# Optimization experiments

Hardware: AMD Instinct MI355X
Metric: run time of the kernel (lower is better)

## Reference

```python
import jax, jax.numpy as jnp
import numpy as np

B, N, NE = 16, 96, 256
ATOM, EDIM, HID, LAT, HEADS = 128, 16, 128, 128, 4
HD = LAT // HEADS
RBF, CUT, ZEMB, MAXZ = 16, 5.0, 32, 100
MUL0_IN, MUL1_IN = 64, 32      # irreps_node = 64x0e + 32x1o (dim 160)
MUL0_OUT, MUL1_OUT = 32, 16    # out irreps  = 32x0e + 16x1o (dim 80)
NODE_DIM = MUL0_IN + 3 * MUL1_IN
OUT_DIM = MUL0_OUT + 3 * MUL1_OUT
E_ATT = 1024
WNUM = MUL0_IN*MUL0_OUT + MUL0_IN*MUL1_OUT + MUL1_IN*MUL1_OUT + MUL1_IN*MUL0_OUT  # 4608


def _mlp3(x, w1, b1, w2, b2, w3, b3):
    x = jax.nn.silu(x @ w1 + b1)
    x = jax.nn.silu(x @ w2 + b2)
    return x @ w3 + b3


def setup_inputs() -> dict:
    key = jax.random.key(0)
    ks = jax.random.split(key, 40)
    s = 0.05  # scale params so deep MLP activations stay numerically sane
    d = {}
    d['h'] = jax.random.normal(ks[0], (B, N, ATOM), jnp.float32)
    d['h_full'] = jax.random.normal(ks[1], (B, N, NODE_DIM), jnp.float32)
    d['e_feat'] = jax.random.normal(ks[2], (NE, EDIM), jnp.float32)
    d['att_dist'] = jax.random.uniform(ks[3], (E_ATT,), jnp.float32)
    d['att_vec'] = jax.random.normal(ks[4], (E_ATT, 3), jnp.float32)
    d['z_emb_table'] = jax.random.normal(ks[5], (MAXZ + 1, ZEMB), jnp.float32) * s
    d['rw1'] = jax.random.normal(ks[6], (ZEMB + 1 + RBF, HID), jnp.float32) * s
    d['rb1'] = jnp.zeros((HID,), jnp.float32)
    d['rw2'] = jax.random.normal(ks[7], (HID, WNUM), jnp.float32) * s
    d['rb2'] = jnp.zeros((WNUM,), jnp.float32)
    d['ew1'] = jax.random.normal(ks[8], (EDIM, HID), jnp.float32) * s
    d['eb1'] = jnp.zeros((HID,), jnp.float32)
    d['ew2'] = jax.random.normal(ks[9], (HID, MUL0_OUT + MUL1_OUT), jnp.float32) * s
    d['eb2'] = jnp.zeros((MUL0_OUT + MUL1_OUT,), jnp.float32)
    d['qw1'] = jax.random.normal(ks[10], (ATOM + EDIM, HID), jnp.float32) * s
    d['qb1'] = jnp.zeros((HID,), jnp.float32)
    d['qw2'] = jax.random.normal(ks[11], (HID, HID), jnp.float32) * s
    d['qb2'] = jnp.zeros((HID,), jnp.float32)
    d['qw3'] = jax.random.normal(ks[12], (HID, LAT), jnp.float32) * s
    d['qb3'] = jnp.zeros((LAT,), jnp.float32)
    d['kw1'] = jax.random.normal(ks[13], (ATOM + ZEMB + 1 + RBF, HID), jnp.float32) * s
    d['kb1'] = jnp.zeros((HID,), jnp.float32)
    d['kw2'] = jax.random.normal(ks[14], (HID, HID), jnp.float32) * s
    d['kb2'] = jnp.zeros((HID,), jnp.float32)
    d['kw3'] = jax.random.normal(ks[15], (HID, LAT), jnp.float32) * s
    d['kb3'] = jnp.zeros((LAT,), jnp.float32)
    d['ow1'] = jax.random.normal(ks[16], (MUL0_OUT + MUL1_OUT, HID), jnp.float32) * s
    d['ob1'] = jnp.zeros((HID,), jnp.float32)
    d['ow2'] = jax.random.normal(ks[17], (HID, HID), jnp.float32) * s
    d['ob2'] = jnp.zeros((HID,), jnp.float32)
    d['ow3'] = jax.random.normal(ks[18], (HID, LAT), jnp.float32) * s
    d['ob3'] = jnp.zeros((LAT,), jnp.float32)
    d['z'] = jax.random.randint(ks[19], (B, N), 0, MAXZ)
    d['mask'] = jnp.ones((B, N), bool)
    d['absorber_index'] = jax.random.randint(ks[20], (B,), 0, N)
    d['att_dst'] = jnp.arange(E_ATT)  # unique flat indices into B*N
    return d


def reference(h, h_full, e_feat, att_dist, att_vec, z_emb_table,
              rw1, rb1, rw2, rb2, ew1, eb1, ew2, eb2,
              qw1, qb1, qw2, qb2, qw3, qb3,
              kw1, kb1, kw2, kb2, kw3, kb3,
              ow1, ob1, ow2, ob2, ow3, ob3,
              z, mask, absorber_index, att_dst):
    Bz, Na, Hd = h.shape
    F = Bz * Na
    nE = e_feat.shape[0]
    # scatter edge data into flat (B*N) atom slots
    am_flat = jnp.zeros((F,), bool).at[att_dst].set(True)
    d_flat = jnp.zeros((F,), h.dtype).at[att_dst].set(att_dist)
    v_flat = jnp.zeros((F, 3), h.dtype).at[att_dst].set(att_vec)
    att_mask = am_flat.reshape(Bz, Na) & mask
    # spherical harmonics (lmax=1, component normalization): Y0 = 1, Y1 = sqrt(3)*unit_vec
    un = v_flat / jnp.maximum(jnp.linalg.norm(v_flat, axis=-1, keepdims=True), 1e-8)
    y1 = jnp.sqrt(3.0) * un
    # Gaussian RBF on absorber->atom distance
    mu = jnp.linspace(0.0, CUT, RBF)
    delta = CUT / (RBF - 1)
    rbf = jnp.exp(-(d_flat[:, None] - mu) ** 2 / (2.0 * delta * delta))  # (F, RBF)
    zr = z_emb_table[z]                      # (B, N, ZEMB)
    zr_flat = zr.reshape(F, -1)
    is_abs = jnp.zeros((Bz, Na), h.dtype).at[jnp.arange(Bz), absorber_index].set(1.0)
    # radial MLP -> per-edge tensor-product weights
    w_in = jnp.concatenate([zr_flat, is_abs.reshape(F, 1), rbf], -1)
    tpw = jax.nn.silu(w_in @ rw1 + rb1) @ rw2 + rb2  # (F, WNUM)
    s1 = MUL0_IN * MUL0_OUT
    s2 = s1 + MUL0_IN * MUL1_OUT
    s3 = s2 + MUL1_IN * MUL1_OUT
    w00 = tpw[:, :s1].reshape(F, MUL0_IN, MUL0_OUT)   # 0e x 0e -> 0e
    w01 = tpw[:, s1:s2].reshape(F, MUL0_IN, MUL1_OUT) # 0e x 1o -> 1o
    w10 = tpw[:, s2:s3].reshape(F, MUL1_IN, MUL1_OUT) # 1o x 0e -> 1o
    w11 = tpw[:, s3:].reshape(F, MUL1_IN, MUL0_OUT)   # 1o x 1o -> 0e
    hf = h_full.reshape(F, -1)
    x0 = hf[:, :MUL0_IN]
    x1 = hf[:, MUL0_IN:].reshape(F, MUL1_IN, 3)
    alpha = 1.0 / jnp.sqrt(jnp.float32(MUL0_IN + MUL1_IN))  # path fan-in normalization
    c = 1.0 / jnp.sqrt(3.0)                                  # wigner-3j coeff for l=1 couplings
    out0 = alpha * (jnp.einsum('fi,fio->fo', x0, w00)
                    + c * jnp.einsum('fim,fm,fio->fo', x1, y1, w11))
    out1 = alpha * c * (jnp.einsum('fi,fm,fio->fom', x0, y1, w01)
                        + jnp.einsum('fim,fio->fom', x1, w10))
    v_irrep = jnp.concatenate([out0, out1.reshape(F, 3 * MUL1_OUT)], -1)  # (F, OUT_DIM)
    # cosine cutoff envelope + edge mask
    env = jnp.where(d_flat < CUT, 0.5 * (jnp.cos(jnp.pi * d_flat / CUT) + 1.0), 0.0)
    v_irrep = v_irrep * (am_flat.astype(h.dtype) * env)[:, None]
    # energy-conditioned per-irrep-channel modulation
    gates = jax.nn.silu(e_feat @ ew1 + eb1) @ ew2 + eb2  # (nE, 48)
    g_exp = jnp.concatenate([gates[:, :MUL0_OUT],
                             jnp.repeat(gates[:, MUL0_OUT:], 3, axis=-1)], -1)  # (nE, OUT_DIM)
    v_mod = (v_irrep[:, None, :] * g_exp[None]).reshape(Bz, Na, nE, OUT_DIM)
    # invariant multi-head scoring
    h_abs = h[jnp.arange(Bz), absorber_index]  # (B, H)
    q_in = jnp.concatenate([jnp.broadcast_to(h_abs[:, None], (Bz, nE, Hd)),
                            jnp.broadcast_to(e_feat[None], (Bz, nE, EDIM))], -1)
    q = _mlp3(q_in, qw1, qb1, qw2, qb2, qw3, qb3)  # (B, nE, LAT)
    atom_static = jnp.concatenate([h, zr, is_abs[..., None], rbf.reshape(Bz, Na, RBF)], -1)
    k = _mlp3(atom_static, kw1, kb1, kw2, kb2, kw3, kb3)  # (B, N, LAT)
    qh = q.reshape(Bz, nE, HEADS, HD)
    kh = k.reshape(Bz, Na, HEADS, HD)
    scores = (jnp.einsum('behd,bnhd->benh', qh, kh) * (HD ** -0.5)).mean(-1)  # (B, nE, N)
    m = att_mask[:, None, :]
    scores = jnp.where(m, scores, -1e9)
    attn = jax.nn.softmax(scores, axis=2) * m.astype(h.dtype)
    attn = attn / jnp.maximum(attn.sum(2, keepdims=True), 1e-8)
    out_irrep = jnp.einsum('ben,bnec->bec', attn, v_mod)  # (B, nE, OUT_DIM)
    # invariants: scalars + vector norms
    scal = out_irrep[..., :MUL0_OUT]
    vec = out_irrep[..., MUL0_OUT:].reshape(Bz, nE, MUL1_OUT, 3)
    inv = jnp.concatenate([scal, jnp.sqrt(jnp.sum(vec * vec, -1) + 1e-12)], -1)
    return _mlp3(inv, ow1, ob1, ow2, ob2, ow3, ob3)  # (B, nE, LAT)
```

## Files before the change

### kernel.cpp

```cpp
#include <hip/hip_runtime.h>
#include <hip/hip_fp16.h>
#include <math.h>

#define BB 16
#define NN 96
#define NE 256
#define FF (BB*NN)
#define ATOM 128
#define EDIM 16
#define HID 128
#define LAT 128
#define RBFN 16
#define CUTOFF 5.0f
#define ZEMB 32
#define E_ATT 1024
#define M0I 64
#define M1I 32
#define M0O 32
#define M1O 16
#define NODE_DIM 160
#define OUT_DIM 80
#define INVD 48
#define WNUM 4608
#define SEG1 2048
#define SEG2 3072
#define SEG3 3584

#define NODE_BLKS (FF/4)
#define EC_BLKS 16
#define HABS_BLKS 2
#define GATE_BLKS 16
#define TRANS_BLKS 144
#define STAGE1_BLKS (NODE_BLKS + EC_BLKS + HABS_BLKS + GATE_BLKS + TRANS_BLKS)

#define MFMA_BLKS (36*16)
#define MQ_BLKS (MFMA_BLKS + 512)

#define SCORE_BLKS 128
#define ST_BLKS (SCORE_BLKS + 512)

typedef _Float16 half8_t __attribute__((ext_vector_type(8)));
typedef float float4v __attribute__((ext_vector_type(4)));

__device__ __forceinline__ float silu_f(float x) { return x / (1.0f + expf(-x)); }

__global__ __launch_bounds__(1024) void k_prep(
    const int* __restrict__ att_dst, const float* __restrict__ att_dist,
    const float* __restrict__ att_vec,
    int* __restrict__ inv, float* __restrict__ y1E, float* __restrict__ envE)
{
    int t = threadIdx.x;
    inv[t] = -1;
    if (t < FF - 1024) inv[1024 + t] = -1;
    {
        float d = att_dist[t];
        envE[t] = (d < CUTOFF) ? 0.5f*(cosf(3.14159265358979323846f*d/CUTOFF) + 1.0f) : 0.0f;
        float vx = att_vec[3*t], vy = att_vec[3*t+1], vz = att_vec[3*t+2];
        float nrm = sqrtf(vx*vx + vy*vy + vz*vz);
        float is = 1.0f / fmaxf(nrm, 1e-8f);
        const float s3 = 1.7320508075688772f;
        y1E[3*t]   = s3*vx*is;
        y1E[3*t+1] = s3*vy*is;
        y1E[3*t+2] = s3*vz*is;
    }
    __syncthreads();
    inv[att_dst[t]] = t;
}

__global__ __launch_bounds__(256) void k_stage1(
    const float* __restrict__ h, const float* __restrict__ z_emb, const int* __restrict__ z,
    const int* __restrict__ absorber, const float* __restrict__ e_feat,
    const int* __restrict__ inv, const float* __restrict__ att_dist,
    const float* __restrict__ rw1, const float* __restrict__ rb1,
    const float* __restrict__ kw1, const float* __restrict__ kb1,
    const float* __restrict__ kw2, const float* __restrict__ kb2,
    const float* __restrict__ kw3, const float* __restrict__ kb3,
    const float* __restrict__ qw1,
    const float* __restrict__ ew1, const float* __restrict__ eb1,
    const float* __restrict__ ew2, const float* __restrict__ eb2,
    const float* __restrict__ rw2,
    __half* __restrict__ hiddenH, float* __restrict__ kmatw,
    float* __restrict__ ecw, float* __restrict__ habs1w, float* __restrict__ gexp,
    __half* __restrict__ rw2T)
{
    __shared__ float smem[3488];
    int blk = blockIdx.x;
    int t = threadIdx.x;

    if (blk < NODE_BLKS) {
        float (*sin1)[184] = (float(*)[184])smem;
        float (*l1S)[128]  = (float(*)[128])(smem + 736);
        float (*l2S)[128]  = (float(*)[128])(smem + 736 + 512);
        int f0 = blk * 4;
        {
            int n = t >> 6, i2 = t & 63;
            float2 hv = *(const float2*)&h[(f0 + n)*ATOM + i2*2];
            sin1[n][i2*2] = hv.x; sin1[n][i2*2 + 1] = hv.y;
        }
        if (t < 128) {
            int n = t >> 5, j = t & 31;
            sin1[n][ATOM + j] = z_emb[z[f0 + n]*ZEMB + j];
        }
        if (t < 64) {
            int n = t >> 4, j = t & 15;
            int e = inv[f0 + n];
            float d = ((unsigned)e < E_ATT) ? att_dist[e] : 0.0f;
            const float delta = CUTOFF / (RBFN - 1);
            float diff = d - j*delta;
            sin1[n][ATOM + ZEMB + 1 + j] = expf(-diff*diff / (2.0f*delta*delta));
        }
        if (t < 4) {
            int f = f0 + t;
            int b = f / NN, nn = f - b*NN;
            sin1[t][ATOM + ZEMB] = (absorber[b] == nn) ? 1.0f : 0.0f;
        }
        __syncthreads();
        int n = t >> 6;
        int c2 = (t & 63) * 2;
        int e = inv[f0 + n];
        bool att_ = ((unsigned)e < E_ATT);
        if (att_) {
            float2 a0 = *(const float2*)&rb1[c2];
            float2 a1 = make_float2(0.f, 0.f);
            #pragma unroll 8
            for (int i = 0; i < 48; i += 2) {
                float x0v = sin1[n][ATOM + i], x1v = sin1[n][ATOM + i + 1];
                float2 w0 = *(const float2*)&rw1[i*HID + c2];
                float2 w1 = *(const float2*)&rw1[(i+1)*HID + c2];
                a0.x += x0v*w0.x; a0.y += x0v*w0.y;
                a1.x += x1v*w1.x; a1.y += x1v*w1.y;
            }
            {
                float x0v = sin1[n][ATOM + 48];
                float2 w0 = *(const float2*)&rw1[48*HID + c2];
                a0.x += x0v*w0.x; a0.y += x0v*w0.y;
            }
            *(__half2*)&hiddenH[e*HID + c2] =
                __floats2half2_rn(silu_f(a0.x + a1.x), silu_f(a0.y + a1.y));
        }
        if (att_) {
            float2 a0 = *(const float2*)&kb1[c2];
            float2 a1 = make_float2(0.f, 0.f);
            #pragma unroll 8
            for (int i = 0; i < 176; i += 2) {
                float x0v = sin1[n][i], x1v = sin1[n][i + 1];
                float2 w0 = *(const float2*)&kw1[i*HID + c2];
                float2 w1 = *(const float2*)&kw1[(i+1)*HID + c2];
                a0.x += x0v*w0.x; a0.y += x0v*w0.y;
                a1.x += x1v*w1.x; a1.y += x1v*w1.y;
            }
            {
                float x0v = sin1[n][176];
                float2 w0 = *(const float2*)&kw1[176*HID + c2];
                a0.x += x0v*w0.x; a0.y += x0v*w0.y;
            }
            l1S[n][c2] = silu_f(a0.x + a1.x); l1S[n][c2+1] = silu_f(a0.y + a1.y);
        }
        __syncthreads();
        if (att_) {
            float2 a0 = *(const float2*)&kb2[c2];
            float2 a1 = make_float2(0.f, 0.f);
            #pragma unroll 8
            for (int i = 0; i < HID; i += 2) {
                float x0v = l1S[n][i], x1v = l1S[n][i + 1];
                float2 w0 = *(const float2*)&kw2[i*HID + c2];
                float2 w1 = *(const float2*)&kw2[(i+1)*HID + c2];
                a0.x += x0v*w0.x; a0.y += x0v*w0.y;
                a1.x += x1v*w1.x; a1.y += x1v*w1.y;
            }
            l2S[n][c2] = silu_f(a0.x + a1.x); l2S[n][c2+1] = silu_f(a0.y + a1.y);
        }
        __syncthreads();
        if (att_) {
            float2 a0 = *(const float2*)&kb3[c2];
            float2 a1 = make_float2(0.f, 0.f);
            #pragma unroll 8
            for (int i = 0; i < HID; i += 2) {
                float x0v = l2S[n][i], x1v = l2S[n][i + 1];
                float2 w0 = *(const float2*)&kw3[i*HID + c2];
                float2 w1 = *(const float2*)&kw3[(i+1)*HID + c2];
                a0.x += x0v*w0.x; a0.y += x0v*w0.y;
                a1.x += x1v*w1.x; a1.y += x1v*w1.y;
            }
            float2 o; o.x = a0.x + a1.x; o.y = a0.y + a1.y;
            *(float2*)&kmatw[(f0 + n)*HID + c2] = o;
        }
    } else if (blk < NODE_BLKS + EC_BLKS) {
        float (*ef)[16] = (float(*)[16])smem;
        int e0 = (blk - NODE_BLKS) * 16;
        { int e = t >> 4, i = t & 15; ef[e][i] = e_feat[(e0 + e)*EDIM + i]; }
        __syncthreads();
        int r = t >> 4, c0 = (t & 15)*8;
        float4 a0 = make_float4(0,0,0,0), a1 = a0;
        #pragma unroll
        for (int i = 0; i < EDIM; i++) {
            float a = ef[r][i];
            float4 w0 = *(const float4*)&qw1[(ATOM + i)*HID + c0];
            float4 w1 = *(const float4*)&qw1[(ATOM + i)*HID + c0 + 4];
            a0.x += a*w0.x; a0.y += a*w0.y; a0.z += a*w0.z; a0.w += a*w0.w;
            a1.x += a*w1.x; a1.y += a*w1.y; a1.z += a*w1.z; a1.w += a*w1.w;
        }
        *(float4*)&ecw[(e0 + r)*HID + c0] = a0;
        *(float4*)&ecw[(e0 + r)*HID + c0 + 4] = a1;
    } else if (blk < NODE_BLKS + EC_BLKS + HABS_BLKS) {
        float (*hr)[128] = (float(*)[128])smem;
        int b0 = (blk - NODE_BLKS - EC_BLKS) * 8;
        {
            int r = t >> 5, i4 = t & 31;
            int b = b0 + r;
            int a = absorber[b];
            *(float4*)&hr[r][i4*4] = *(const float4*)&h[(b*NN + a)*ATOM + i4*4];
        }
        __syncthreads();
        int r = t >> 5, c0 = (t & 31)*4;
        float4 a0 = make_float4(0,0,0,0), a1 = a0;
        #pragma unroll 8
        for (int i = 0; i < ATOM; i += 2) {
            float x0v = hr[r][i], x1v = hr[r][i+1];
            float4 w0 = *(const float4*)&qw1[i*HID + c0];
            float4 w1 = *(const float4*)&qw1[(i+1)*HID + c0];
            a0.x += x0v*w0.x; a0.y += x0v*w0.y; a0.z += x0v*w0.z; a0.w += x0v*w0.w;
            a1.x += x1v*w1.x; a1.y += x1v*w1.y; a1.z += x1v*w1.z; a1.w += x1v*w1.w;
        }
        float4 o;
        o.x = a0.x + a1.x; o.y = a0.y + a1.y; o.z = a0.z + a1.z; o.w = a0.w + a1.w;
        *(float4*)&habs1w[(b0 + r)*HID + c0] = o;
    } else if (blk < NODE_BLKS + EC_BLKS + HABS_BLKS + GATE_BLKS) {
        float (*ef)[16]   = (float(*)[16])smem;
        float (*l1g)[128] = (float(*)[128])(smem + 256);
        float (*gg)[48]   = (float(*)[48])(smem + 256 + 2048);
        int e0 = (blk - NODE_BLKS - EC_BLKS - HABS_BLKS) * 16;
        { int e = t >> 4, i = t & 15; ef[e][i] = e_feat[(e0 + e)*EDIM + i]; }
        __syncthreads();
        int r = t >> 4, c0 = (t & 15)*8;
        {
            float4 a0 = *(const float4*)&eb1[c0];
            float4 a1 = *(const float4*)&eb1[c0 + 4];
            #pragma unroll
            for (int i = 0; i < EDIM; i++) {
                float a = ef[r][i];
                float4 w0 = *(const float4*)&ew1[i*HID + c0];
                float4 w1 = *(const float4*)&ew1[i*HID + c0 + 4];
                a0.x += a*w0.x; a0.y += a*w0.y; a0.z += a*w0.z; a0.w += a*w0.w;
                a1.x += a*w1.x; a1.y += a*w1.y; a1.z += a*w1.z; a1.w += a*w1.w;
            }
            l1g[r][c0]   = silu_f(a0.x); l1g[r][c0+1] = silu_f(a0.y);
            l1g[r][c0+2] = silu_f(a0.z); l1g[r][c0+3] = silu_f(a0.w);
            l1g[r][c0+4] = silu_f(a1.x); l1g[r][c0+5] = silu_f(a1.y);
            l1g[r][c0+6] = silu_f(a1.z); l1g[r][c0+7] = silu_f(a1.w);
        }
        __syncthreads();
        for (int u = t; u < 16*48; u += 256) {
            int e = u / 48, j = u - 48*(u/48);
            float acc = eb2[j];
            #pragma unroll 4
            for (int i = 0; i < HID; i++) acc += l1g[e][i]*ew2[i*48 + j];
            gg[e][j] = acc;
        }
        __syncthreads();
        for (int u = t; u < 16*80; u += 256) {
            int e = u / 80, cc = u - 80*(u/80);
            gexp[(e0 + e)*OUT_DIM + cc] = (cc < M0O) ? gg[e][cc] : gg[e][M0O + (cc - M0O)/3];
        }
    } else {
        __half* lds = (__half*)smem;
        int tb = blk - (NODE_BLKS + EC_BLKS + HABS_BLKS + GATE_BLKS);
        int nt = tb % 72, kt = tb / 72;
        int n0 = nt*64, k0 = kt*64;
        for (int p = 0; p < 16; p++) {
            int idx = t + 256*p;
            int kk = idx >> 6, nn = idx & 63;
            lds[nn*66 + kk] = __float2half(rw2[(k0+kk)*WNUM + n0+nn]);
        }
        __syncthreads();
        for (int p = 0; p < 16; p++) {
            int idx = t + 256*p;
            int nn = idx >> 6, kk = idx & 63;
            rw2T[(n0+nn)*HID + k0+kk] = lds[nn*66 + kk];
        }
    }
}

__global__ __launch_bounds__(256) void k_mq(
    const __half* __restrict__ hiddenH, const __half* __restrict__ rw2T,
    const float* __restrict__ rb2,
    const float* __restrict__ habs1, const float* __restrict__ ec, const float* __restrict__ qb1,
    const float* __restrict__ qw2, const float* __restrict__ qb2,
    const float* __restrict__ qw3, const float* __restrict__ qb3,
    __half* __restrict__ tpwE, float* __restrict__ qmat)
{
    __shared__ __align__(16) char smemraw[17408];
    int blk = blockIdx.x;
    int t = threadIdx.x;
    if (blk < MFMA_BLKS) {
        int colTile = blk % 36;
        int rowGrp  = blk / 36;
        int wv = t >> 6;
        int lane = t & 63;
        int m0 = (rowGrp*4 + wv) * 16;
        int n0 = colTile * 128;
        int mrow = lane & 15, quad = lane >> 4;
        __half* cS = (__half*)smemraw + wv * (16*136);
        const _Float16* hp = (const _Float16*)hiddenH + (m0 + mrow)*HID + quad*8;
        half8_t af[4];
        #pragma unroll
        for (int kc = 0; kc < 4; kc++) af[kc] = *(const half8_t*)(hp + kc*32);
        #pragma unroll
        for (int nt = 0; nt < 8; nt++) {
            const _Float16* bp = (const _Float16*)rw2T + (n0 + nt*16 + mrow)*HID + quad*8;
            float4v acc = {0.f, 0.f, 0.f, 0.f};
            #pragma unroll
            for (int kc = 0; kc < 4; kc++) {
                half8_t bf = *(const half8_t*)(bp + kc*32);
                acc = __builtin_amdgcn_mfma_f32_16x16x32_f16(af[kc], bf, acc, 0, 0, 0);
            }
            float bias = rb2[n0 + nt*16 + mrow];
            #pragma unroll
            for (int r = 0; r < 4; r++)
                cS[(quad*4 + r)*136 + nt*16 + mrow] = __float2half(acc[r] + bias);
        }
        #pragma unroll
        for (int p = 0; p < 4; p++) {
            int chunk = lane + 64*p;
            int row = chunk >> 4, c8 = (chunk & 15)*8;
            float4 v = *(float4*)&cS[row*136 + c8];
            *(float4*)&tpwE[(long)(m0 + row)*WNUM + n0 + c8] = v;
        }
    } else {
        float* l1S = (float*)smemraw;
        float* l2S = (float*)smemraw + 1024;
        int r0 = (blk - MFMA_BLKS) * 8;
        for (int p = 0; p < 4; p++) {
            int idx = t + 256*p;
            int rr = idx >> 7, i = idx & 127;
            int be = r0 + rr; int b = be >> 8; int e = be & 255;
            l1S[rr*128 + i] = silu_f(habs1[b*HID + i] + ec[e*HID + i] + qb1[i]);
        }
        __syncthreads();
        int r = t >> 5, c0 = (t & 31)*4;
        {
            float4 a0 = *(const float4*)&qb2[c0];
            float4 a1 = make_float4(0,0,0,0);
            #pragma unroll 8
            for (int i = 0; i < HID; i += 2) {
                float x0v = l1S[r*128 + i], x1v = l1S[r*128 + i+1];
                float4 w0 = *(const float4*)&qw2[i*HID + c0];
                float4 w1 = *(const float4*)&qw2[(i+1)*HID + c0];
                a0.x += x0v*w0.x; a0.y += x0v*w0.y; a0.z += x0v*w0.z; a0.w += x0v*w0.w;
                a1.x += x1v*w1.x; a1.y += x1v*w1.y; a1.z += x1v*w1.z; a1.w += x1v*w1.w;
            }
            l2S[r*128 + c0]   = silu_f(a0.x + a1.x); l2S[r*128 + c0+1] = silu_f(a0.y + a1.y);
            l2S[r*128 + c0+2] = silu_f(a0.z + a1.z); l2S[r*128 + c0+3] = silu_f(a0.w + a1.w);
        }
        __syncthreads();
        {
            float4 a0 = *(const float4*)&qb3[c0];
            float4 a1 = make_float4(0,0,0,0);
            #pragma unroll 8
            for (int i = 0; i < HID; i += 2) {
                float x0v = l2S[r*128 + i], x1v = l2S[r*128 + i+1];
                float4 w0 = *(const float4*)&qw3[i*HID + c0];
                float4 w1 = *(const float4*)&qw3[(i+1)*HID + c0];
                a0.x += x0v*w0.x; a0.y += x0v*w0.y; a0.z += x0v*w0.z; a0.w += x0v*w0.w;
                a1.x += x1v*w1.x; a1.y += x1v*w1.y; a1.z += x1v*w1.z; a1.w += x1v*w1.w;
            }
            float4 o;
            o.x = a0.x + a1.x; o.y = a0.y + a1.y; o.z = a0.z + a1.z; o.w = a0.w + a1.w;
            *(float4*)&qmat[(r0 + r)*LAT + c0] = o;
        }
    }
}

__global__ __launch_bounds__(256) void k_st(
    const float* __restrict__ qmat, const float* __restrict__ kmat, const int* __restrict__ inv,
    const float* __restrict__ h_full, const __half* __restrict__ tpwE,
    const int* __restrict__ att_dst,
    const float* __restrict__ envE, const float* __restrict__ y1E,
    float* __restrict__ scoresW, float* __restrict__ virr)
{
    __shared__ float smem[8544];
    int blk = blockIdx.x;
    int t = threadIdx.x;
    if (blk < SCORE_BLKS) {
        int b  = blk >> 3;
        int e0 = (blk & 7) * 32;
        float (*Qs)[132] = (float(*)[132])smem;
        float (*Kt)[132] = (float(*)[132])(smem + 32*132);
        float* mS = smem + 2*32*132;
        for (int p = 0; p < 4; p++) {
            int idx = t + 256*p; int e = idx >> 5, i4 = idx & 31;
            *(float4*)&Qs[e][i4*4] = *(const float4*)&qmat[(b*NE + e0 + e)*LAT + i4*4];
        }
        if (t < NN) mS[t] = ((unsigned)inv[b*NN + t] < E_ATT) ? 1.0f : 0.0f;
        int te = t >> 5, tn = t & 31;
        float acc[4][3] = {};
        for (int nt = 0; nt < 3; nt++) {
            __syncthreads();
            for (int p = 0; p < 4; p++) {
                int idx = t + 256*p; int n = idx >> 5, i4 = idx & 31;
                *(float4*)&Kt[n][i4*4] = *(const float4*)&kmat[(b*NN + nt*32 + n)*LAT + i4*4];
            }
            __syncthreads();
            for (int i = 0; i < LAT; i++) {
                float bv = Kt[tn][i];
                acc[0][nt] += Qs[te*4 + 0][i]*bv;
                acc[1][nt] += Qs[te*4 + 1][i]*bv;
                acc[2][nt] += Qs[te*4 + 2][i]*bv;
                acc[3][nt] += Qs[te*4 + 3][i]*bv;
            }
        }
        const float scale = 0.04419417382415922f;
        #pragma unroll
        for (int j = 0; j < 4; j++)
            #pragma unroll
            for (int jj = 0; jj < 3; jj++) {
                int n = tn + 32*jj;
                float s = (mS[n] != 0.f) ? acc[j][jj]*scale : -1e9f;
                scoresW[((b*NE) + e0 + te*4 + j)*NN + n] = s;
            }
    } else {
        int sub = t >> 7, tt = t & 127;
        int e = (blk - SCORE_BLKS)*2 + sub;
        int f = att_dst[e];
        float* x0  = smem + sub*256;
        float* x1f = smem + sub*256 + 64;
        float* xy  = smem + sub*256 + 160;
        float* y1s = smem + sub*256 + 192;
        const float* hf = h_full + f*NODE_DIM;
        if (tt < M0I) x0[tt] = hf[tt];
        if (tt < M1I*3) x1f[tt] = hf[M0I + tt];
        if (tt < 3) y1s[tt] = y1E[3*e + tt];
        __syncthreads();
        if (tt < M1I) xy[tt] = x1f[3*tt]*y1s[0] + x1f[3*tt+1]*y1s[1] + x1f[3*tt+2]*y1s[2];
        __syncthreads();
        float scale = envE[e];
        const __half* w = tpwE + (long)e*WNUM;
        const float alpha = 0.10206207261596575f;
        const float cc = 0.5773502691896258f;
        if (tt < M0O) {
            float t00 = 0.f, t11 = 0.f;
            #pragma unroll 4
            for (int i = 0; i < M0I; i++) t00 += x0[i]*__half2float(w[i*M0O + tt]);
            #pragma unroll 4
            for (int i = 0; i < M1I; i++) t11 += xy[i]*__half2float(w[SEG3 + i*M0O + tt]);
            virr[f*OUT_DIM + tt] = alpha*(t00 + cc*t11)*scale;
        } else if (tt < M0O + 3*M1O) {
            int idx = tt - M0O; int o = idx/3, m = idx - 3*o;
            float t01 = 0.f, t10 = 0.f;
            #pragma unroll 4
            for (int i = 0; i < M0I; i++) t01 += x0[i]*__half2float(w[SEG1 + i*M1O + o]);
            #pragma unroll 4
            for (int i = 0; i < M1I; i++) t10 += x1f[i*3 + m]*__half2float(w[SEG2 + i*M1O + o]);
            virr[f*OUT_DIM + tt] = alpha*cc*(t01*y1s[m] + t10)*scale;
        }
    }
}

__global__ __launch_bounds__(256) void k_attf(
    const float* __restrict__ scoresW, const int* __restrict__ inv,
    const float* __restrict__ virr, const float* __restrict__ gexp,
    const float* __restrict__ ow1, const float* __restrict__ ob1,
    const float* __restrict__ ow2, const float* __restrict__ ob2,
    const float* __restrict__ ow3, const float* __restrict__ ob3,
    float* __restrict__ out)
{
    int b  = blockIdx.x >> 5;
    int e0 = (blockIdx.x & 31) * 8;
    int t = threadIdx.x;
    __shared__ float aS[8][100];
    __shared__ float gS[8][84];
    __shared__ float ocS[8][84];
    __shared__ float mS[NN];
    __shared__ float inS[8][INVD];
    __shared__ float l1S[8][HID];
    __shared__ float l2S[8][HID];

    for (int p = 0; p < 3; p++) {
        int idx = t + 256*p;
        int el = idx / NN, n = idx - NN*(idx/NN);
        aS[el][n] = scoresW[((b*NE) + e0 + el)*NN + n];
    }
    if (t < 160) {
        int el = t / 20, c4 = t - 20*(t/20);
        *(float4*)&gS[el][c4*4] = *(const float4*)&gexp[(e0 + el)*OUT_DIM + c4*4];
    }
    if (t < NN) mS[t] = ((unsigned)inv[b*NN + t] < E_ATT) ? 1.0f : 0.0f;
    __syncthreads();

    {
        int el = t >> 5;
        int ng = t & 31;
        float s0 = aS[el][ng], s1 = aS[el][ng + 32], s2 = aS[el][ng + 64];
        float m0 = mS[ng], m1 = mS[ng + 32], m2 = mS[ng + 64];
        float mx = fmaxf(s0, fmaxf(s1, s2));
        #pragma unroll
        for (int off = 1; off < 32; off <<= 1) mx = fmaxf(mx, __shfl_xor(mx, off));
        float e0v = expf(s0 - mx), e1v = expf(s1 - mx), e2v = expf(s2 - mx);
        float sm = e0v + e1v + e2v;
        #pragma unroll
        for (int off = 1; off < 32; off <<= 1) sm += __shfl_xor(sm, off);
        float r = 1.0f / sm;
        float p0 = m0*e0v*r, p1 = m1*e1v*r, p2 = m2*e2v*r;
        float ss = p0 + p1 + p2;
        #pragma unroll
        for (int off = 1; off < 32; off <<= 1) ss += __shfl_xor(ss, off);
        float is = 1.0f / fmaxf(ss, 1e-8f);
        aS[el][ng]      = p0*is;
        aS[el][ng + 32] = p1*is;
        aS[el][ng + 64] = p2*is;
    }
    __syncthreads();

    if (t < 160) {
        int el = t / 20, c4 = t - 20*(t/20);
        const float* vp = virr + (long)b*NN*OUT_DIM + c4*4;
        float4 acc = make_float4(0,0,0,0);
        #pragma unroll 4
        for (int n = 0; n < NN; n++) {
            float a = aS[el][n];
            float4 v = *(const float4*)&vp[n*OUT_DIM];
            acc.x += a*v.x; acc.y += a*v.y; acc.z += a*v.z; acc.w += a*v.w;
        }
        float4 g = *(float4*)&gS[el][c4*4];
        float4 o; o.x = acc.x*g.x; o.y = acc.y*g.y; o.z = acc.z*g.z; o.w = acc.w*g.w;
        *(float4*)&ocS[el][c4*4] = o;
    }
    __syncthreads();

    for (int u = t; u < 8*INVD; u += 256) {
        int el = u / INVD, j = u - INVD*(u/INVD);
        float val;
        if (j < M0O) val = ocS[el][j];
        else {
            int o = j - M0O;
            float x = ocS[el][M0O + 3*o], y = ocS[el][M0O + 3*o + 1], zz = ocS[el][M0O + 3*o + 2];
            val = sqrtf(x*x + y*y + zz*zz + 1e-12f);
        }
        inS[el][j] = val;
    }
    __syncthreads();

    int r = t >> 5, c0 = (t & 31)*4;
    {
        float4 a0 = *(const float4*)&ob1[c0];
        float4 a1 = make_float4(0,0,0,0);
        #pragma unroll 8
        for (int i = 0; i < INVD; i += 2) {
            float x0v = inS[r][i], x1v = inS[r][i+1];
            float4 w0 = *(const float4*)&ow1[i*HID + c0];
            float4 w1 = *(const float4*)&ow1[(i+1)*HID + c0];
            a0.x += x0v*w0.x; a0.y += x0v*w0.y; a0.z += x0v*w0.z; a0.w += x0v*w0.w;
            a1.x += x1v*w1.x; a1.y += x1v*w1.y; a1.z += x1v*w1.z; a1.w += x1v*w1.w;
        }
        l1S[r][c0]   = silu_f(a0.x + a1.x); l1S[r][c0+1] = silu_f(a0.y + a1.y);
        l1S[r][c0+2] = silu_f(a0.z + a1.z); l1S[r][c0+3] = silu_f(a0.w + a1.w);
    }
    __syncthreads();
    {
        float4 a0 = *(const float4*)&ob2[c0];
        float4 a1 = make_float4(0,0,0,0);
        #pragma unroll 8
        for (int i = 0; i < HID; i += 2) {
            float x0v = l1S[r][i], x1v = l1S[r][i+1];
            float4 w0 = *(const float4*)&ow2[i*HID + c0];
            float4 w1 = *(const float4*)&ow2[(i+1)*HID + c0];
            a0.x += x0v*w0.x; a0.y += x0v*w0.y; a0.z += x0v*w0.z; a0.w += x0v*w0.w;
            a1.x += x1v*w1.x; a1.y += x1v*w1.y; a1.z += x1v*w1.z; a1.w += x1v*w1.w;
        }
        l2S[r][c0]   = silu_f(a0.x + a1.x); l2S[r][c0+1] = silu_f(a0.y + a1.y);
        l2S[r][c0+2] = silu_f(a0.z + a1.z); l2S[r][c0+3] = silu_f(a0.w + a1.w);
    }
    __syncthreads();
    {
        float4 a0 = *(const float4*)&ob3[c0];
        float4 a1 = make_float4(0,0,0,0);
        #pragma unroll 8
        for (int i = 0; i < HID; i += 2) {
            float x0v = l2S[r][i], x1v = l2S[r][i+1];
            float4 w0 = *(const float4*)&ow3[i*HID + c0];
            float4 w1 = *(const float4*)&ow3[(i+1)*HID + c0];
            a0.x += x0v*w0.x; a0.y += x0v*w0.y; a0.z += x0v*w0.z; a0.w += x0v*w0.w;
            a1.x += x1v*w1.x; a1.y += x1v*w1.y; a1.z += x1v*w1.z; a1.w += x1v*w1.w;
        }
        float4 o;
        o.x = a0.x + a1.x; o.y = a0.y + a1.y; o.z = a0.z + a1.z; o.w = a0.w + a1.w;
        *(float4*)&out[((b*NE + e0) + r)*LAT + c0] = o;
    }
}

extern "C" void kernel_launch(void* const* d_in, const int* in_sizes, int n_in,
                              void* d_out, int out_size, void* d_ws, size_t ws_size,
                              hipStream_t stream) {
    const float* h        = (const float*)d_in[0];
    const float* h_full   = (const float*)d_in[1];
    const float* e_feat   = (const float*)d_in[2];
    const float* att_dist = (const float*)d_in[3];
    const float* att_vec  = (const float*)d_in[4];
    const float* z_emb    = (const float*)d_in[5];
    const float* rw1 = (const float*)d_in[6];  const float* rb1 = (const float*)d_in[7];
    const float* rw2 = (const float*)d_in[8];  const float* rb2 = (const float*)d_in[9];
    const float* ew1 = (const float*)d_in[10]; const float* eb1 = (const float*)d_in[11];
    const float* ew2 = (const float*)d_in[12]; const float* eb2 = (const float*)d_in[13];
    const float* qw1 = (const float*)d_in[14]; const float* qb1 = (const float*)d_in[15];
    const float* qw2 = (const float*)d_in[16]; const float* qb2 = (const float*)d_in[17];
    const float* qw3 = (const float*)d_in[18]; const float* qb3 = (const float*)d_in[19];
    const float* kw1 = (const float*)d_in[20]; const float* kb1 = (const float*)d_in[21];
    const float* kw2 = (const float*)d_in[22]; const float* kb2 = (const float*)d_in[23];
    const float* kw3 = (const float*)d_in[24]; const float* kb3 = (const float*)d_in[25];
    const float* ow1 = (const float*)d_in[26]; const float* ob1 = (const float*)d_in[27];
    const float* ow2 = (const float*)d_in[28]; const float* ob2 = (const float*)d_in[29];
    const float* ow3 = (const float*)d_in[30]; const float* ob3 = (const float*)d_in[31];
    const int* z        = (const int*)d_in[32];
    const int* absorber = (const int*)d_in[34];
    const int* att_dst  = (const int*)d_in[35];

    float* ws = (float*)d_ws;
    int*   inv     = (int*)ws;
    float* y1E     = ws + 1536;
    float* envE    = ws + 4608;
    float* kmat    = ws + 5632;
    float* qmat    = ws + 202240;
    float* gexp    = ws + 726528;
    float* virr    = ws + 747008;
    float* habs1   = ws + 869888;
    float* ec      = ws + 871936;
    float* scoresW = ws + 904704;
    __half* tpwE   = (__half*)(ws + 1297920);
    __half* rw2T   = (__half*)(ws + 3657216);
    __half* hiddenH= (__half*)(ws + 3952128);

    float* out = (float*)d_out;

    k_prep<<<1, 1024, 0, stream>>>(att_dst, att_dist, att_vec, inv, y1E, envE);
    k_stage1<<<STAGE1_BLKS, 256, 0, stream>>>(h, z_emb, z, absorber, e_feat, inv, att_dist,
                                              rw1, rb1, kw1, kb1, kw2, kb2, kw3, kb3,
                                              qw1, ew1, eb1, ew2, eb2, rw2,
                                              hiddenH, kmat, ec, habs1, gexp, rw2T);
    k_mq<<<MQ_BLKS, 256, 0, stream>>>(hiddenH, rw2T, rb2, habs1, ec, qb1,
                                      qw2, qb2, qw3, qb3, tpwE, qmat);
    k_st<<<ST_BLKS, 256, 0, stream>>>(qmat, kmat, inv, h_full, tpwE, att_dst,
                                      envE, y1E, scoresW, virr);
    k_attf<<<BB*32, 256, 0, stream>>>(scoresW, inv, virr, gexp,
                                      ow1, ob1, ow2, ob2, ow3, ob3, out);
}
```

Before: 237.0 us.

## Fold prep kernel into stage1 and index node MLP work by attention edge

Removes the separate single-block k_prep launch and moves its work (inverse index init, envelope and unit-vector computation) into an extra block of k_stage1. Node blocks are now indexed by attention edge via att_dst rather than by node with an inverse lookup. Only nodes that are edge destinations are processed, so the 1536-node grid with many idle nodes shrinks to 256 blocks with no inactive warps. This relies on att_dst being unique; duplicate destinations would write kmat twice.

```diff
diff --git a/kernel.cpp b/kernel.cpp
--- a/kernel.cpp
+++ b/kernel.cpp
@@ -26,12 +26,13 @@
 #define SEG2 3072
 #define SEG3 3584
 
-#define NODE_BLKS (FF/4)
+#define EDGE_BLKS (E_ATT/4)
 #define EC_BLKS 16
 #define HABS_BLKS 2
 #define GATE_BLKS 16
 #define TRANS_BLKS 144
-#define STAGE1_BLKS (NODE_BLKS + EC_BLKS + HABS_BLKS + GATE_BLKS + TRANS_BLKS)
+#define PREP_BLKS 1
+#define STAGE1_BLKS (EDGE_BLKS + EC_BLKS + HABS_BLKS + GATE_BLKS + TRANS_BLKS + PREP_BLKS)
 
 #define MFMA_BLKS (36*16)
 #define MQ_BLKS (MFMA_BLKS + 512)
@@ -43,34 +44,12 @@
 typedef float float4v __attribute__((ext_vector_type(4)));
 
 __device__ __forceinline__ float silu_f(float x) { return x / (1.0f + expf(-x)); }
-
-__global__ __launch_bounds__(1024) void k_prep(
-    const int* __restrict__ att_dst, const float* __restrict__ att_dist,
-    const float* __restrict__ att_vec,
-    int* __restrict__ inv, float* __restrict__ y1E, float* __restrict__ envE)
-{
-    int t = threadIdx.x;
-    inv[t] = -1;
-    if (t < FF - 1024) inv[1024 + t] = -1;
-    {
-        float d = att_dist[t];
-        envE[t] = (d < CUTOFF) ? 0.5f*(cosf(3.14159265358979323846f*d/CUTOFF) + 1.0f) : 0.0f;
-        float vx = att_vec[3*t], vy = att_vec[3*t+1], vz = att_vec[3*t+2];
-        float nrm = sqrtf(vx*vx + vy*vy + vz*vz);
-        float is = 1.0f / fmaxf(nrm, 1e-8f);
-        const float s3 = 1.7320508075688772f;
-        y1E[3*t]   = s3*vx*is;
-        y1E[3*t+1] = s3*vy*is;
-        y1E[3*t+2] = s3*vz*is;
-    }
-    __syncthreads();
-    inv[att_dst[t]] = t;
-}
 
 __global__ __launch_bounds__(256) void k_stage1(
     const float* __restrict__ h, const float* __restrict__ z_emb, const int* __restrict__ z,
     const int* __restrict__ absorber, const float* __restrict__ e_feat,
-    const int* __restrict__ inv, const float* __restrict__ att_dist,
+    const int* __restrict__ att_dst, const float* __restrict__ att_dist,
+    const float* __restrict__ att_vec,
     const float* __restrict__ rw1, const float* __restrict__ rb1,
     const float* __restrict__ kw1, const float* __restrict__ kb1,
     const float* __restrict__ kw2, const float* __restrict__ kb2,
@@ -81,113 +60,106 @@
     const float* __restrict__ rw2,
     __half* __restrict__ hiddenH, float* __restrict__ kmatw,
     float* __restrict__ ecw, float* __restrict__ habs1w, float* __restrict__ gexp,
-    __half* __restrict__ rw2T)
+    __half* __restrict__ rw2T,
+    int* __restrict__ inv, float* __restrict__ y1E, float* __restrict__ envE)
 {
     __shared__ float smem[3488];
     int blk = blockIdx.x;
     int t = threadIdx.x;
 
-    if (blk < NODE_BLKS) {
+    if (blk < EDGE_BLKS) {
         float (*sin1)[184] = (float(*)[184])smem;
         float (*l1S)[128]  = (float(*)[128])(smem + 736);
         float (*l2S)[128]  = (float(*)[128])(smem + 736 + 512);
-        int f0 = blk * 4;
-        {
-            int n = t >> 6, i2 = t & 63;
-            float2 hv = *(const float2*)&h[(f0 + n)*ATOM + i2*2];
-            sin1[n][i2*2] = hv.x; sin1[n][i2*2 + 1] = hv.y;
-        }
-        if (t < 128) {
-            int n = t >> 5, j = t & 31;
-            sin1[n][ATOM + j] = z_emb[z[f0 + n]*ZEMB + j];
-        }
-        if (t < 64) {
-            int n = t >> 4, j = t & 15;
-            int e = inv[f0 + n];
-            float d = ((unsigned)e < E_ATT) ? att_dist[e] : 0.0f;
+        int w = t >> 6;
+        int c = t & 63;
+        int e = blk*4 + w;
+        int f = att_dst[e];
+        int b = f / NN, nn = f - b*NN;
+        float d = att_dist[e];
+        {
+            float2 hv = *(const float2*)&h[f*ATOM + 2*c];
+            sin1[w][2*c] = hv.x; sin1[w][2*c + 1] = hv.y;
+        }
+        if (c < ZEMB) sin1[w][ATOM + c] = z_emb[z[f]*ZEMB + c];
+        if (c >= 32 && c < 48) {
+            int j = c - 32;
             const float delta = CUTOFF / (RBFN - 1);
             float diff = d - j*delta;
-            sin1[n][ATOM + ZEMB + 1 + j] = expf(-diff*diff / (2.0f*delta*delta));
-        }
-        if (t < 4) {
-            int f = f0 + t;
-            int b = f / NN, nn = f - b*NN;
-            sin1[t][ATOM + ZEMB] = (absorber[b] == nn) ? 1.0f : 0.0f;
-        }
-        __syncthreads();
-        int n = t >> 6;
-        int c2 = (t & 63) * 2;
-        int e = inv[f0 + n];
-        bool att_ = ((unsigned)e < E_ATT);
-        if (att_) {
+            sin1[w][ATOM + ZEMB + 1 + j] = expf(-diff*diff / (2.0f*delta*delta));
+        }
+        if (c == 48) sin1[w][ATOM + ZEMB] = (absorber[b] == nn) ? 1.0f : 0.0f;
+        __syncthreads();
+        int c2 = 2*c;
+        {
             float2 a0 = *(const float2*)&rb1[c2];
             float2 a1 = make_float2(0.f, 0.f);
             #pragma unroll 8
             for (int i = 0; i < 48; i += 2) {
-                float x0v = sin1[n][ATOM + i], x1v = sin1[n][ATOM + i + 1];
+                float x0v = sin1[w][ATOM + i], x1v = sin1[w][ATOM + i + 1];
                 float2 w0 = *(const float2*)&rw1[i*HID + c2];
                 float2 w1 = *(const float2*)&rw1[(i+1)*HID + c2];
                 a0.x += x0v*w0.x; a0.y += x0v*w0.y;
                 a1.x += x1v*w1.x; a1.y += x1v*w1.y;
             }
             {
-                float x0v = sin1[n][ATOM + 48];
+                float x0v = sin1[w][ATOM + 48];
                 float2 w0 = *(const float2*)&rw1[48*HID + c2];
                 a0.x += x0v*w0.x; a0.y += x0v*w0.y;
             }
             *(__half2*)&hiddenH[e*HID + c2] =
                 __floats2half2_rn(silu_f(a0.x + a1.x), silu_f(a0.y + a1.y));
         }
-        if (att_) {
+        {
             float2 a0 = *(const float2*)&kb1[c2];
             float2 a1 = make_float2(0.f, 0.f);
             #pragma unroll 8
             for (int i = 0; i < 176; i += 2) {
-                float x0v = sin1[n][i], x1v = sin1[n][i + 1];
+                float x0v = sin1[w][i], x1v = sin1[w][i + 1];
                 float2 w0 = *(const float2*)&kw1[i*HID + c2];
                 float2 w1 = *(const float2*)&kw1[(i+1)*HID + c2];
                 a0.x += x0v*w0.x; a0.y += x0v*w0.y;
                 a1.x += x1v*w1.x; a1.y += x1v*w1.y;
             }
             {
-                float x0v = sin1[n][176];
+                float x0v = sin1[w][176];
                 float2 w0 = *(const float2*)&kw1[176*HID + c2];
                 a0.x += x0v*w0.x; a0.y += x0v*w0.y;
             }
-            l1S[n][c2] = silu_f(a0.x + a1.x); l1S[n][c2+1] = silu_f(a0.y + a1.y);
-        }
-        __syncthreads();
-        if (att_) {
+            l1S[w][c2] = silu_f(a0.x + a1.x); l1S[w][c2+1] = silu_f(a0.y + a1.y);
+        }
+        __syncthreads();
+        {
             float2 a0 = *(const float2*)&kb2[c2];
             float2 a1 = make_float2(0.f, 0.f);
             #pragma unroll 8
             for (int i = 0; i < HID; i += 2) {
-                float x0v = l1S[n][i], x1v = l1S[n][i + 1];
+                float x0v = l1S[w][i], x1v = l1S[w][i + 1];
                 float2 w0 = *(const float2*)&kw2[i*HID + c2];
                 float2 w1 = *(const float2*)&kw2[(i+1)*HID + c2];
                 a0.x += x0v*w0.x; a0.y += x0v*w0.y;
                 a1.x += x1v*w1.x; a1.y += x1v*w1.y;
             }
-            l2S[n][c2] = silu_f(a0.x + a1.x); l2S[n][c2+1] = silu_f(a0.y + a1.y);
-        }
-        __syncthreads();
-        if (att_) {
+            l2S[w][c2] = silu_f(a0.x + a1.x); l2S[w][c2+1] = silu_f(a0.y + a1.y);
+        }
+        __syncthreads();
+        {
             float2 a0 = *(const float2*)&kb3[c2];
             float2 a1 = make_float2(0.f, 0.f);
             #pragma unroll 8
             for (int i = 0; i < HID; i += 2) {
-                float x0v = l2S[n][i], x1v = l2S[n][i + 1];
+                float x0v = l2S[w][i], x1v = l2S[w][i + 1];
                 float2 w0 = *(const float2*)&kw3[i*HID + c2];
                 float2 w1 = *(const float2*)&kw3[(i+1)*HID + c2];
                 a0.x += x0v*w0.x; a0.y += x0v*w0.y;
                 a1.x += x1v*w1.x; a1.y += x1v*w1.y;
             }
             float2 o; o.x = a0.x + a1.x; o.y = a0.y + a1.y;
-            *(float2*)&kmatw[(f0 + n)*HID + c2] = o;
-        }
-    } else if (blk < NODE_BLKS + EC_BLKS) {
+            *(float2*)&kmatw[f*HID + c2] = o;
+        }
+    } else if (blk < EDGE_BLKS + EC_BLKS) {
         float (*ef)[16] = (float(*)[16])smem;
-        int e0 = (blk - NODE_BLKS) * 16;
+        int e0 = (blk - EDGE_BLKS) * 16;
         { int e = t >> 4, i = t & 15; ef[e][i] = e_feat[(e0 + e)*EDIM + i]; }
         __syncthreads();
         int r = t >> 4, c0 = (t & 15)*8;
@@ -202,9 +174,9 @@
         }
         *(float4*)&ecw[(e0 + r)*HID + c0] = a0;
         *(float4*)&ecw[(e0 + r)*HID + c0 + 4] = a1;
-    } else if (blk < NODE_BLKS + EC_BLKS + HABS_BLKS) {
+    } else if (blk < EDGE_BLKS + EC_BLKS + HABS_BLKS) {
         float (*hr)[128] = (float(*)[128])smem;
-        int b0 = (blk - NODE_BLKS - EC_BLKS) * 8;
+        int b0 = (blk - EDGE_BLKS - EC_BLKS) * 8;
         {
             int r = t >> 5, i4 = t & 31;
             int b = b0 + r;
@@ -225,11 +197,11 @@
         float4 o;
         o.x = a0.x + a1.x; o.y = a0.y + a1.y; o.z = a0.z + a1.z; o.w = a0.w + a1.w;
         *(float4*)&habs1w[(b0 + r)*HID + c0] = o;
-    } else if (blk < NODE_BLKS + EC_BLKS + HABS_BLKS + GATE_BLKS) {
+    } else if (blk < EDGE_BLKS + EC_BLKS + HABS_BLKS + GATE_BLKS) {
         float (*ef)[16]   = (float(*)[16])smem;
         float (*l1g)[128] = (float(*)[128])(smem + 256);
         float (*gg)[48]   = (float(*)[48])(smem + 256 + 2048);
-        int e0 = (blk - NODE_BLKS - EC_BLKS - HABS_BLKS) * 16;
+        int e0 = (blk - EDGE_BLKS - EC_BLKS - HABS_BLKS) * 16;
         { int e = t >> 4, i = t & 15; ef[e][i] = e_feat[(e0 + e)*EDIM + i]; }
         __syncthreads();
         int r = t >> 4, c0 = (t & 15)*8;
@@ -262,9 +234,9 @@
             int e = u / 80, cc = u - 80*(u/80);
             gexp[(e0 + e)*OUT_DIM + cc] = (cc < M0O) ? gg[e][cc] : gg[e][M0O + (cc - M0O)/3];
         }
-    } else {
+    } else if (blk < EDGE_BLKS + EC_BLKS + HABS_BLKS + GATE_BLKS + TRANS_BLKS) {
         __half* lds = (__half*)smem;
-        int tb = blk - (NODE_BLKS + EC_BLKS + HABS_BLKS + GATE_BLKS);
+        int tb = blk - (EDGE_BLKS + EC_BLKS + HABS_BLKS + GATE_BLKS);
         int nt = tb % 72, kt = tb / 72;
         int n0 = nt*64, k0 = kt*64;
         for (int p = 0; p < 16; p++) {
@@ -278,6 +250,22 @@
             int nn = idx >> 6, kk = idx & 63;
             rw2T[(n0+nn)*HID + k0+kk] = lds[nn*66 + kk];
         }
+    } else {
+        for (int p = 0; p < 6; p++) inv[t + 256*p] = -1;
+        for (int p = 0; p < 4; p++) {
+            int e = t + 256*p;
+            float d = att_dist[e];
+            envE[e] = (d < CUTOFF) ? 0.5f*(cosf(3.14159265358979323846f*d/CUTOFF) + 1.0f) : 0.0f;
+            float vx = att_vec[3*e], vy = att_vec[3*e+1], vz = att_vec[3*e+2];
+            float nrm = sqrtf(vx*vx + vy*vy + vz*vz);
+            float is = 1.0f / fmaxf(nrm, 1e-8f);
+            const float s3 = 1.7320508075688772f;
+            y1E[3*e]   = s3*vx*is;
+            y1E[3*e+1] = s3*vy*is;
+            y1E[3*e+2] = s3*vz*is;
+        }
+        __syncthreads();
+        for (int p = 0; p < 4; p++) { int e = t + 256*p; inv[att_dst[e]] = e; }
     }
 }
 
@@ -631,11 +619,12 @@
 
     float* out = (float*)d_out;
 
-    k_prep<<<1, 1024, 0, stream>>>(att_dst, att_dist, att_vec, inv, y1E, envE);
-    k_stage1<<<STAGE1_BLKS, 256, 0, stream>>>(h, z_emb, z, absorber, e_feat, inv, att_dist,
+    k_stage1<<<STAGE1_BLKS, 256, 0, stream>>>(h, z_emb, z, absorber, e_feat,
+                                              att_dst, att_dist, att_vec,
                                               rw1, rb1, kw1, kb1, kw2, kb2, kw3, kb3,
                                               qw1, ew1, eb1, ew2, eb2, rw2,
-                                              hiddenH, kmat, ec, habs1, gexp, rw2T);
+                                              hiddenH, kmat, ec, habs1, gexp, rw2T,
+                                              inv, y1E, envE);
     k_mq<<<MQ_BLKS, 256, 0, stream>>>(hiddenH, rw2T, rb2, habs1, ec, qb1,
                                       qw2, qb2, qw3, qb3, tpwE, qmat);
     k_st<<<ST_BLKS, 256, 0, stream>>>(qmat, kmat, inv, h_full, tpwE, att_dst,
```

After: 236.8 us (median of 2 runs). About the same (-0.1%).
